# Kernel optimization log

Measured on AMD Instinct MI355X. Metric: run time of the kernel, lower is better.

## Reference

```python
import jax, jax.numpy as jnp
import numpy as np

D_IN = 1024
D_EMB = 512
HIDDEN = 256
NUM_CLASSES = 64
N_SUPPORT = 4096
N_QUERY = 8192


def setup_inputs() -> dict:
    key = jax.random.key(0)
    ks = jax.random.split(key, 8)
    scale_e = 1.0 / np.sqrt(D_IN)
    scale_1 = 1.0 / np.sqrt(2 * D_EMB)
    scale_2 = 1.0 / np.sqrt(HIDDEN)
    return {
        "support_data": jax.random.normal(ks[0], (N_SUPPORT, D_IN), jnp.float32),
        "query_data": jax.random.normal(ks[1], (N_QUERY, D_IN), jnp.float32),
        "support_label": jax.random.randint(ks[2], (N_SUPPORT,), 0, NUM_CLASSES, jnp.int32),
        "W_e": jax.random.normal(ks[3], (D_IN, D_EMB), jnp.float32) * scale_e,
        "b_e": jnp.zeros((D_EMB,), jnp.float32),
        "W1": jax.random.normal(ks[4], (2 * D_EMB, HIDDEN), jnp.float32) * scale_1,
        "b1": jnp.zeros((HIDDEN,), jnp.float32),
        "W2": jax.random.normal(ks[5], (HIDDEN, 1), jnp.float32) * scale_2,
        "b2": jnp.zeros((1,), jnp.float32),
    }


def reference(support_data, query_data, support_label, W_e, b_e, W1, b1, W2, b2):
    # embedding_net: Linear + ReLU
    s_emb = jax.nn.relu(support_data @ W_e + b_e)  # [Ns, D_EMB]
    q_emb = jax.nn.relu(query_data @ W_e + b_e)    # [Nq, D_EMB]

    # per-class mean of support embeddings (segment mean; labels are 0..C-1,
    # matching torch.unique()'s sorted order)
    sums = jax.ops.segment_sum(s_emb, support_label, num_segments=NUM_CLASSES)
    counts = jax.ops.segment_sum(jnp.ones((s_emb.shape[0],), s_emb.dtype),
                                 support_label, num_segments=NUM_CLASSES)
    means = sums / jnp.maximum(counts, 1.0)[:, None]  # [C, D_EMB]

    # relation_net on concat(query, class_mean): split first linear so the
    # [Nq*C, 2*D_EMB] concat is never materialized (same math).
    Wq, Wc = W1[:D_EMB], W1[D_EMB:]
    h = jax.nn.relu(q_emb @ Wq[:, None, :].squeeze(1) @ jnp.eye(HIDDEN, dtype=W1.dtype)
                    if False else
                    (q_emb @ Wq)[:, None, :] + (means @ Wc)[None, :, :] + b1)  # [Nq, C, HIDDEN]
    scores = jax.nn.sigmoid(h @ W2 + b2)  # [Nq, C, 1]
    # torch version stacks [1,1]-shaped scores -> [Nq, C, 1, 1]
    return scores[:, :, None, :]
```

## Files before the change

kernel.cpp:

```cpp
#include <hip/hip_runtime.h>
#include <hip/hip_bf16.h>

#define D_IN 1024
#define D_EMB 512
#define HIDDEN 256
#define NUM_CLASSES 64
#define N_SUPPORT 4096
#define N_QUERY 8192

typedef __bf16 bf16x8 __attribute__((ext_vector_type(8)));
typedef __bf16 bf16x4 __attribute__((ext_vector_type(4)));
typedef float f32x4 __attribute__((ext_vector_type(4)));

#define GLOAD_LDS16(g, l)                                                          \
  __builtin_amdgcn_global_load_lds(                                                \
      (const __attribute__((address_space(1))) unsigned int*)(g),                  \
      (__attribute__((address_space(3))) unsigned int*)(l), 16, 0, 0)

__global__ __launch_bounds__(256) void prep(
    const float* __restrict__ W_e, const float* __restrict__ W1,
    const float* __restrict__ support, const float* __restrict__ query,
    __bf16* __restrict__ WeT, __bf16* __restrict__ WqT,
    __bf16* __restrict__ Xbf) {
  const int tid = threadIdx.x;
  int b = blockIdx.x;
  if (b < 640) {
    __shared__ float tile[32][33];
    const float* in;
    __bf16* out;
    int bx, by, rows, cols;
    if (b < 512) {
      in = W_e; out = WeT; rows = D_IN; cols = D_EMB;
      bx = (b & 15) * 32; by = (b >> 4) * 32;
    } else {
      b -= 512;
      in = W1; out = WqT; rows = D_EMB; cols = HIDDEN;
      bx = (b & 7) * 32; by = (b >> 3) * 32;
    }
    int tx = tid & 31, ty = tid >> 5;
#pragma unroll
    for (int i = ty; i < 32; i += 8)
      tile[i][tx] = in[(long)(by + i) * cols + bx + tx];
    __syncthreads();
#pragma unroll
    for (int i = ty; i < 32; i += 8)
      out[(long)(bx + i) * rows + by + tx] = (__bf16)tile[tx][i];
  } else {
    const long nsup = (long)N_SUPPORT * D_IN;
    long base = (long)(b - 640) * 4096;
#pragma unroll
    for (int g = 0; g < 4; ++g) {
      long i = base + g * 1024 + tid * 4;
      const float* src = (i < nsup) ? (support + i) : (query + (i - nsup));
      float4 v = *(const float4*)src;
      bf16x4 o;
      o[0] = (__bf16)v.x; o[1] = (__bf16)v.y;
      o[2] = (__bf16)v.z; o[3] = (__bf16)v.w;
      *(bf16x4*)(Xbf + i) = o;
    }
  }
}

__global__ __launch_bounds__(256, 3) void gemm_emb(
    const __bf16* __restrict__ A, const __bf16* __restrict__ BT,
    const float* __restrict__ bias, __bf16* __restrict__ C) {
  constexpr int BM = 128, BN = 64, BK = 32;
  constexpr int N = D_EMB, K = D_IN;
  constexpr int NT = K / BK;
  constexpr int MR = 4, NR = 2;

  __shared__ __align__(16) __bf16 As[4][BM * BK];
  __shared__ __align__(16) __bf16 Bs[4][BN * BK];

  const int tid = threadIdx.x;
  const int wave = tid >> 6, lane = tid & 63;
  const int wr = wave >> 1, wc = wave & 1;
  const int l16 = lane & 15, half = lane >> 4;
  const int slot = half ^ ((l16 >> 1) & 3);

  const int m0 = blockIdx.x * BM;
  const int n0 = blockIdx.y * BN;

  const int ar0 = tid >> 2;
  const int ak0 = (tid & 3) ^ ((ar0 >> 1) & 3);
  const int ar1 = (tid + 256) >> 2;
  const int ak1 = (tid & 3) ^ ((ar1 >> 1) & 3);
  const __bf16* aptr0 = A + (long)(m0 + ar0) * K + ak0 * 8;
  const __bf16* aptr1 = A + (long)(m0 + ar1) * K + ak1 * 8;
  const int brow = tid >> 2;
  const int bkc = (tid & 3) ^ ((brow >> 1) & 3);
  const __bf16* bptr = BT + (long)(n0 + brow) * K + bkc * 8;

  f32x4 acc[MR][NR];
#pragma unroll
  for (int m = 0; m < MR; ++m)
#pragma unroll
    for (int n = 0; n < NR; ++n) acc[m][n] = (f32x4)0.0f;

#define STAGE(t, buf)                                                       \
  {                                                                         \
    GLOAD_LDS16(aptr0 + (t) * BK, &As[buf][tid * 8]);                       \
    GLOAD_LDS16(aptr1 + (t) * BK, &As[buf][(tid + 256) * 8]);               \
    GLOAD_LDS16(bptr + (t) * BK, &Bs[buf][tid * 8]);                        \
  }

#define COMPUTE(buf)                                                        \
  {                                                                         \
    bf16x8 a[MR], b[NR];                                                    \
    _Pragma("unroll") for (int m = 0; m < MR; ++m)                          \
        a[m] = *(const bf16x8*)(&As[buf][(wr * 64 + m * 16 + l16) * BK +    \
                                         slot * 8]);                        \
    _Pragma("unroll") for (int n = 0; n < NR; ++n)                          \
        b[n] = *(const bf16x8*)(&Bs[buf][(wc * 32 + n * 16 + l16) * BK +    \
                                         slot * 8]);                        \
    asm volatile("s_waitcnt lgkmcnt(0)" ::: "memory");                      \
    __builtin_amdgcn_sched_barrier(0);                                      \
    _Pragma("unroll") for (int m = 0; m < MR; ++m)                          \
        _Pragma("unroll") for (int n = 0; n < NR; ++n)                      \
            acc[m][n] = __builtin_amdgcn_mfma_f32_16x16x32_bf16(            \
                a[m], b[n], acc[m][n], 0, 0, 0);                            \
  }

  STAGE(0, 0);
  STAGE(1, 1);
  STAGE(2, 2);
  asm volatile("s_waitcnt vmcnt(6)" ::: "memory");
  __builtin_amdgcn_s_barrier();

  for (int t = 0; t < NT - 3; ++t) {
    STAGE(t + 3, (t + 3) & 3);
    COMPUTE(t & 3);
    asm volatile("s_waitcnt vmcnt(6)" ::: "memory");
    __builtin_amdgcn_s_barrier();
  }
  COMPUTE((NT - 3) & 3);
  asm volatile("s_waitcnt vmcnt(3)" ::: "memory");
  __builtin_amdgcn_s_barrier();
  COMPUTE((NT - 2) & 3);
  asm volatile("s_waitcnt vmcnt(0)" ::: "memory");
  __builtin_amdgcn_s_barrier();
  COMPUTE((NT - 1) & 3);

#undef STAGE
#undef COMPUTE

#pragma unroll
  for (int m = 0; m < MR; ++m)
#pragma unroll
    for (int n = 0; n < NR; ++n) {
      const int col = n0 + wc * 32 + n * 16 + l16;
      const float bv = bias[col];
#pragma unroll
      for (int j = 0; j < 4; ++j) {
        int row = m0 + wr * 64 + m * 16 + half * 4 + j;
        float v = fmaxf(acc[m][n][j] + bv, 0.0f);
        C[(long)row * N + col] = (__bf16)v;
      }
    }
}

__global__ __launch_bounds__(256, 4) void qp_proto(
    const __bf16* __restrict__ emb, const __bf16* __restrict__ BT,
    const float* __restrict__ bias, float* __restrict__ Cqp,
    const int* __restrict__ labels, float* __restrict__ sums_part,
    int* __restrict__ cnt_part) {
  constexpr int BM = 64, BN = 64, BK = 32;
  constexpr int N = HIDDEN, K = D_EMB;
  constexpr int NT = K / BK;
  constexpr int MR = 2, NR = 2;

  __shared__ __align__(16) __bf16 As[4][BM * BK];
  __shared__ __align__(16) __bf16 Bs[4][BN * BK];

  const int tid = threadIdx.x;
  const int bid = blockIdx.x;

  if (bid >= 512) {
    const int pb = bid - 512;
    const int c = pb >> 3;
    const int s = pb & 7;
    const int j0 = s * (N_SUPPORT / 8);
    float a0 = 0.0f, a1 = 0.0f;
    int count = 0;
#pragma unroll 4
    for (int j = j0; j < j0 + N_SUPPORT / 8; j += 4) {
      int4 lab4 = *(const int4*)(labels + j);
#pragma unroll
      for (int u = 0; u < 4; ++u) {
        int lab = (u == 0) ? lab4.x : (u == 1) ? lab4.y : (u == 2) ? lab4.z : lab4.w;
        if (lab == c) {
          const __bf16* r = emb + (long)(j + u) * D_EMB;
          a0 += (float)r[tid];
          a1 += (float)r[tid + 256];
          ++count;
        }
      }
    }
    float* dst = sums_part + (long)(c * 8 + s) * D_EMB;
    dst[tid] = a0;
    dst[tid + 256] = a1;
    if (tid == 0) cnt_part[c * 8 + s] = count;
    return;
  }

  const __bf16* A = emb + (long)N_SUPPORT * D_EMB;
  const int wave = tid >> 6, lane = tid & 63;
  const int wr = wave >> 1, wc = wave & 1;
  const int l16 = lane & 15, half = lane >> 4;
  const int slot = half ^ ((l16 >> 1) & 3);

  const int m0 = (bid & 127) * BM;
  const int n0 = (bid >> 7) * BN;

  const int srow = tid >> 2;
  const int skc = (tid & 3) ^ ((srow >> 1) & 3);
  const __bf16* aptr = A + (long)(m0 + srow) * K + skc * 8;
  const __bf16* bptr = BT + (long)(n0 + srow) * K + skc * 8;

  f32x4 acc[MR][NR];
#pragma unroll
  for (int m = 0; m < MR; ++m)
#pragma unroll
    for (int n = 0; n < NR; ++n) acc[m][n] = (f32x4)0.0f;

#define STAGE(t, buf)                                                       \
  {                                                                         \
    GLOAD_LDS16(aptr + (t) * BK, &As[buf][tid * 8]);                        \
    GLOAD_LDS16(bptr + (t) * BK, &Bs[buf][tid * 8]);                        \
  }

#define COMPUTE(buf)                                                        \
  {                                                                         \
    bf16x8 a[MR], b[NR];                                                    \
    _Pragma("unroll") for (int m = 0; m < MR; ++m)                          \
        a[m] = *(const bf16x8*)(&As[buf][(wr * 32 + m * 16 + l16) * BK +    \
                                         slot * 8]);                        \
    _Pragma("unroll") for (int n = 0; n < NR; ++n)                          \
        b[n] = *(const bf16x8*)(&Bs[buf][(wc * 32 + n * 16 + l16) * BK +    \
                                         slot * 8]);                        \
    asm volatile("s_waitcnt lgkmcnt(0)" ::: "memory");                      \
    __builtin_amdgcn_sched_barrier(0);                                      \
    _Pragma("unroll") for (int m = 0; m < MR; ++m)                          \
        _Pragma("unroll") for (int n = 0; n < NR; ++n)                      \
            acc[m][n] = __builtin_amdgcn_mfma_f32_16x16x32_bf16(            \
                a[m], b[n], acc[m][n], 0, 0, 0);                            \
  }

  STAGE(0, 0);
  STAGE(1, 1);
  STAGE(2, 2);
  asm volatile("s_waitcnt vmcnt(4)" ::: "memory");
  __builtin_amdgcn_s_barrier();

  for (int t = 0; t < NT - 3; ++t) {
    STAGE(t + 3, (t + 3) & 3);
    COMPUTE(t & 3);
    asm volatile("s_waitcnt vmcnt(4)" ::: "memory");
    __builtin_amdgcn_s_barrier();
  }
  COMPUTE((NT - 3) & 3);
  asm volatile("s_waitcnt vmcnt(2)" ::: "memory");
  __builtin_amdgcn_s_barrier();
  COMPUTE((NT - 2) & 3);
  asm volatile("s_waitcnt vmcnt(0)" ::: "memory");
  __builtin_amdgcn_s_barrier();
  COMPUTE((NT - 1) & 3);

#undef STAGE
#undef COMPUTE

#pragma unroll
  for (int m = 0; m < MR; ++m)
#pragma unroll
    for (int n = 0; n < NR; ++n) {
      const int col = n0 + wc * 32 + n * 16 + l16;
      const float bv = bias[col];
#pragma unroll
      for (int j = 0; j < 4; ++j) {
        int row = m0 + wr * 32 + m * 16 + half * 4 + j;
        Cqp[(long)row * N + col] = acc[m][n][j] + bv;
      }
    }
}

__global__ __launch_bounds__(256) void proto_cpb(
    const float* __restrict__ sums_part, const int* __restrict__ cnt_part,
    const float* __restrict__ W1, float* __restrict__ cpb_part) {
  __shared__ float ls[128];
  const int c = blockIdx.x;
  const int kc = blockIdx.y;
  const int k0 = kc * 128;
  const int tid = threadIdx.x;

  int nc = 0;
#pragma unroll
  for (int s = 0; s < 8; ++s) nc += cnt_part[c * 8 + s];
  float inv = 1.0f / fmaxf((float)nc, 1.0f);

  if (tid < 128) {
    float v = 0.0f;
#pragma unroll
    for (int s = 0; s < 8; ++s)
      v += sums_part[(long)(c * 8 + s) * D_EMB + k0 + tid];
    ls[tid] = v * inv;
  }
  __syncthreads();

  float acc = 0.0f;
#pragma unroll 8
  for (int k = 0; k < 128; ++k)
    acc = fmaf(ls[k], W1[(long)(D_EMB + k0 + k) * HIDDEN + tid], acc);
  cpb_part[((long)kc * NUM_CLASSES + c) * HIDDEN + tid] = acc;
}

__global__ __launch_bounds__(256) void score_kernel(
    const float* __restrict__ qp, const float* __restrict__ cpb_part,
    const float* __restrict__ W2, const float* __restrict__ b2,
    float* __restrict__ out) {
  constexpr int CPB_S = 260;
  __shared__ __align__(16) float cpb_s[NUM_CLASSES * CPB_S];
  __shared__ __align__(16) float qp_s[32 * HIDDEN];
  __shared__ __align__(16) float w2_s[HIDDEN];

  const int tid = threadIdx.x;
  const int w = tid >> 6;
  const int c = tid & 63;
  const int qb0 = blockIdx.x * 32;
  constexpr int NCH = NUM_CLASSES * HIDDEN;

  w2_s[tid] = W2[tid];
  for (int i = tid; i < NCH; i += 256)
    cpb_s[(i >> 8) * CPB_S + (i & (HIDDEN - 1))] =
        cpb_part[i] + cpb_part[NCH + i] + cpb_part[2 * NCH + i] +
        cpb_part[3 * NCH + i];
  for (int i = tid; i < 32 * HIDDEN; i += 256)
    qp_s[i] = qp[(long)qb0 * HIDDEN + i];
  __syncthreads();

  const float bb = b2[0];
  float acc[8];
#pragma unroll
  for (int q = 0; q < 8; ++q) acc[q] = 0.0f;

  const float* crow = cpb_s + c * CPB_S;
  const float* qbase = qp_s + (w * 8) * HIDDEN;

#pragma unroll 4
  for (int kc = 0; kc < HIDDEN / 4; ++kc) {
    f32x4 cv = *(const f32x4*)(crow + kc * 4);
    f32x4 wv = *(const f32x4*)(w2_s + kc * 4);
#pragma unroll
    for (int q = 0; q < 8; ++q) {
      f32x4 qv = *(const f32x4*)(qbase + q * HIDDEN + kc * 4);
      acc[q] = fmaf(fmaxf(qv[0] + cv[0], 0.0f), wv[0], acc[q]);
      acc[q] = fmaf(fmaxf(qv[1] + cv[1], 0.0f), wv[1], acc[q]);
      acc[q] = fmaf(fmaxf(qv[2] + cv[2], 0.0f), wv[2], acc[q]);
      acc[q] = fmaf(fmaxf(qv[3] + cv[3], 0.0f), wv[3], acc[q]);
    }
  }

#pragma unroll
  for (int q = 0; q < 8; ++q) {
    float x = acc[q] + bb;
    out[(long)(qb0 + w * 8 + q) * NUM_CLASSES + c] = 1.0f / (1.0f + __expf(-x));
  }
}

extern "C" void kernel_launch(void* const* d_in, const int* in_sizes, int n_in,
                              void* d_out, int out_size, void* d_ws,
                              size_t ws_size, hipStream_t stream) {
  const float* support = (const float*)d_in[0];
  const float* query   = (const float*)d_in[1];
  const int*   labels  = (const int*)d_in[2];
  const float* W_e     = (const float*)d_in[3];
  const float* b_e     = (const float*)d_in[4];
  const float* W1      = (const float*)d_in[5];
  const float* b1      = (const float*)d_in[6];
  const float* W2      = (const float*)d_in[7];
  const float* b2      = (const float*)d_in[8];
  float* out = (float*)d_out;

  char* ws = (char*)d_ws;
  size_t off = 0;
  auto alloc = [&](size_t bytes) {
    void* p = ws + off;
    off = (off + bytes + 255) & ~(size_t)255;
    return p;
  };
  const long NTOT = N_SUPPORT + N_QUERY;
  __bf16* Xbf = (__bf16*)alloc((size_t)NTOT * D_IN * 2);
  __bf16* WeT = (__bf16*)alloc((size_t)D_EMB * D_IN * 2);
  __bf16* WqT = (__bf16*)alloc((size_t)HIDDEN * D_EMB * 2);
  __bf16* emb = (__bf16*)alloc((size_t)NTOT * D_EMB * 2);
  float*  qp  = (float*)alloc((size_t)N_QUERY * HIDDEN * 4);
  float*  sums_part = (float*)alloc((size_t)NUM_CLASSES * 8 * D_EMB * 4);
  int*    cnt_part  = (int*)alloc((size_t)NUM_CLASSES * 8 * 4);
  float*  cpb_part  = (float*)alloc((size_t)4 * NUM_CLASSES * HIDDEN * 4);

  prep<<<640 + (int)(NTOT * D_IN / 4096), 256, 0, stream>>>(
      W_e, W1, support, query, WeT, WqT, Xbf);

  gemm_emb<<<dim3(NTOT / 128, D_EMB / 64), 256, 0, stream>>>(
      Xbf, WeT, b_e, emb);

  qp_proto<<<1024, 256, 0, stream>>>(emb, WqT, b1, qp, labels, sums_part,
                                     cnt_part);

  proto_cpb<<<dim3(NUM_CLASSES, 4), 256, 0, stream>>>(sums_part, cnt_part, W1,
                                                      cpb_part);

  score_kernel<<<N_QUERY / 32, 256, 0, stream>>>(qp, cpb_part, W2, b2, out);
}
```

Measured before the change: 87.54 us.

## Switch embedding GEMM to BK=64 double-buffered pipeline with 8-way XOR swizzle

Doubles the K tile of the embedding GEMM to 64 and replaces the 4-stage, 3-deep prefetch pipeline with a 2-buffer ping-pong. The LDS swizzle changes to an 8-chunk XOR pattern, and each COMPUTE issues two k-substeps of MFMAs. The aim is to halve the number of barriers and loop iterations and to give each stage more MFMA work. In exchange, prefetch depth drops to one tile and every iteration waits on vmcnt(0), so global-load latency may be less well hidden.

```diff
diff --git a/kernel.cpp b/kernel.cpp
--- a/kernel.cpp
+++ b/kernel.cpp
@@ -64,32 +64,39 @@
 __global__ __launch_bounds__(256, 3) void gemm_emb(
     const __bf16* __restrict__ A, const __bf16* __restrict__ BT,
     const float* __restrict__ bias, __bf16* __restrict__ C) {
-  constexpr int BM = 128, BN = 64, BK = 32;
+  constexpr int BM = 128, BN = 64, BK = 64;
   constexpr int N = D_EMB, K = D_IN;
   constexpr int NT = K / BK;
   constexpr int MR = 4, NR = 2;
 
-  __shared__ __align__(16) __bf16 As[4][BM * BK];
-  __shared__ __align__(16) __bf16 Bs[4][BN * BK];
+  __shared__ __align__(16) __bf16 As[2][BM * BK];
+  __shared__ __align__(16) __bf16 Bs[2][BN * BK];
 
   const int tid = threadIdx.x;
   const int wave = tid >> 6, lane = tid & 63;
   const int wr = wave >> 1, wc = wave & 1;
   const int l16 = lane & 15, half = lane >> 4;
-  const int slot = half ^ ((l16 >> 1) & 3);
+  const int r7 = l16 & 7;
 
   const int m0 = blockIdx.x * BM;
   const int n0 = blockIdx.y * BN;
 
-  const int ar0 = tid >> 2;
-  const int ak0 = (tid & 3) ^ ((ar0 >> 1) & 3);
-  const int ar1 = (tid + 256) >> 2;
-  const int ak1 = (tid & 3) ^ ((ar1 >> 1) & 3);
-  const __bf16* aptr0 = A + (long)(m0 + ar0) * K + ak0 * 8;
-  const __bf16* aptr1 = A + (long)(m0 + ar1) * K + ak1 * 8;
-  const int brow = tid >> 2;
-  const int bkc = (tid & 3) ^ ((brow >> 1) & 3);
-  const __bf16* bptr = BT + (long)(n0 + brow) * K + bkc * 8;
+  const __bf16* aptr[4];
+#pragma unroll
+  for (int q = 0; q < 4; ++q) {
+    int chunk = q * 256 + tid;
+    int row = chunk >> 3;
+    int kc = (chunk & 7) ^ (row & 7);
+    aptr[q] = A + (long)(m0 + row) * K + kc * 8;
+  }
+  const __bf16* bptr[2];
+#pragma unroll
+  for (int q = 0; q < 2; ++q) {
+    int chunk = q * 256 + tid;
+    int row = chunk >> 3;
+    int kc = (chunk & 7) ^ (row & 7);
+    bptr[q] = BT + (long)(n0 + row) * K + kc * 8;
+  }
 
   f32x4 acc[MR][NR];
 #pragma unroll
@@ -99,47 +106,49 @@
 
 #define STAGE(t, buf)                                                       \
   {                                                                         \
-    GLOAD_LDS16(aptr0 + (t) * BK, &As[buf][tid * 8]);                       \
-    GLOAD_LDS16(aptr1 + (t) * BK, &As[buf][(tid + 256) * 8]);               \
-    GLOAD_LDS16(bptr + (t) * BK, &Bs[buf][tid * 8]);                        \
+    _Pragma("unroll") for (int q = 0; q < 4; ++q)                           \
+        GLOAD_LDS16(aptr[q] + (t) * BK, &As[buf][(q * 256 + tid) * 8]);     \
+    _Pragma("unroll") for (int q = 0; q < 2; ++q)                           \
+        GLOAD_LDS16(bptr[q] + (t) * BK, &Bs[buf][(q * 256 + tid) * 8]);     \
   }
 
 #define COMPUTE(buf)                                                        \
   {                                                                         \
-    bf16x8 a[MR], b[NR];                                                    \
-    _Pragma("unroll") for (int m = 0; m < MR; ++m)                          \
-        a[m] = *(const bf16x8*)(&As[buf][(wr * 64 + m * 16 + l16) * BK +    \
-                                         slot * 8]);                        \
-    _Pragma("unroll") for (int n = 0; n < NR; ++n)                          \
-        b[n] = *(const bf16x8*)(&Bs[buf][(wc * 32 + n * 16 + l16) * BK +    \
-                                         slot * 8]);                        \
+    bf16x8 a[MR][2], b[NR][2];                                              \
+    _Pragma("unroll") for (int m = 0; m < MR; ++m) {                        \
+      int row = wr * 64 + m * 16 + l16;                                     \
+      _Pragma("unroll") for (int ks = 0; ks < 2; ++ks)                      \
+          a[m][ks] = *(const bf16x8*)(&As[buf][row * BK +                   \
+                                      (((ks * 4 + half) ^ r7) * 8)]);       \
+    }                                                                       \
+    _Pragma("unroll") for (int n = 0; n < NR; ++n) {                        \
+      int row = wc * 32 + n * 16 + l16;                                     \
+      _Pragma("unroll") for (int ks = 0; ks < 2; ++ks)                      \
+          b[n][ks] = *(const bf16x8*)(&Bs[buf][row * BK +                   \
+                                      (((ks * 4 + half) ^ r7) * 8)]);       \
+    }                                                                       \
     asm volatile("s_waitcnt lgkmcnt(0)" ::: "memory");                      \
     __builtin_amdgcn_sched_barrier(0);                                      \
-    _Pragma("unroll") for (int m = 0; m < MR; ++m)                          \
-        _Pragma("unroll") for (int n = 0; n < NR; ++n)                      \
-            acc[m][n] = __builtin_amdgcn_mfma_f32_16x16x32_bf16(            \
-                a[m], b[n], acc[m][n], 0, 0, 0);                            \
+    _Pragma("unroll") for (int ks = 0; ks < 2; ++ks)                        \
+        _Pragma("unroll") for (int m = 0; m < MR; ++m)                      \
+            _Pragma("unroll") for (int n = 0; n < NR; ++n)                  \
+                acc[m][n] = __builtin_amdgcn_mfma_f32_16x16x32_bf16(        \
+                    a[m][ks], b[n][ks], acc[m][n], 0, 0, 0);                \
   }
 
   STAGE(0, 0);
-  STAGE(1, 1);
-  STAGE(2, 2);
-  asm volatile("s_waitcnt vmcnt(6)" ::: "memory");
-  __builtin_amdgcn_s_barrier();
-
-  for (int t = 0; t < NT - 3; ++t) {
-    STAGE(t + 3, (t + 3) & 3);
-    COMPUTE(t & 3);
-    asm volatile("s_waitcnt vmcnt(6)" ::: "memory");
-    __builtin_amdgcn_s_barrier();
-  }
-  COMPUTE((NT - 3) & 3);
-  asm volatile("s_waitcnt vmcnt(3)" ::: "memory");
-  __builtin_amdgcn_s_barrier();
-  COMPUTE((NT - 2) & 3);
   asm volatile("s_waitcnt vmcnt(0)" ::: "memory");
   __builtin_amdgcn_s_barrier();
-  COMPUTE((NT - 1) & 3);
+
+  int cur = 0;
+  for (int t = 0; t < NT - 1; ++t) {
+    STAGE(t + 1, cur ^ 1);
+    COMPUTE(cur);
+    asm volatile("s_waitcnt vmcnt(0)" ::: "memory");
+    __builtin_amdgcn_s_barrier();
+    cur ^= 1;
+  }
+  COMPUTE(cur);
 
 #undef STAGE
 #undef COMPUTE
```

Measured after the change: 82.05 us (median of 2 runs). 6.3% less time.
